# Optimization experiments

Hardware: AMD Instinct MI355X
Metric: run time of the kernel (lower is better)

Reference implementation:

```python
import jax, jax.numpy as jnp
import numpy as np

N = 50000      # nodes
E = 800000     # edges
D = 128        # input_dim
H = 128        # hidden_dim
OUT = 86       # output_dim (DDI classes)
P = 100000     # drug pairs
BN_EPS = 1e-5


def setup_inputs() -> dict:
    key = jax.random.key(0)
    ks = jax.random.split(key, 16)
    s = 0.05
    return {
        "x": jax.random.normal(ks[0], (N, D), jnp.float32),
        "edge_index": jax.random.randint(ks[1], (2, E), 0, N),
        "drug_pairs": jax.random.randint(ks[2], (P, 2), 0, N),
        # GCN layer 1 (input_dim -> hidden_dim) + BatchNorm params
        "W1": jax.random.normal(ks[3], (D, H), jnp.float32) * s,
        "b1": jnp.zeros((H,), jnp.float32),
        "gamma1": jnp.ones((H,), jnp.float32),
        "beta1": jnp.zeros((H,), jnp.float32),
        # GCN layer 2 (hidden -> hidden) + BatchNorm params
        "W2": jax.random.normal(ks[4], (H, H), jnp.float32) * s,
        "b2": jnp.zeros((H,), jnp.float32),
        "gamma2": jnp.ones((H,), jnp.float32),
        "beta2": jnp.zeros((H,), jnp.float32),
        # edge classifier MLP: Linear(2H,H) -> ReLU -> Linear(H,H//2) -> ReLU -> Linear(H//2,OUT)
        "Wc1": jax.random.normal(ks[5], (2 * H, H), jnp.float32) * s,
        "bc1": jnp.zeros((H,), jnp.float32),
        "Wc2": jax.random.normal(ks[6], (H, H // 2), jnp.float32) * s,
        "bc2": jnp.zeros((H // 2,), jnp.float32),
        "Wc3": jax.random.normal(ks[7], (H // 2, OUT), jnp.float32) * s,
        "bc3": jnp.zeros((OUT,), jnp.float32),
    }


def gcn_conv(h, W, b, src, dst, n):
    """PyG GCNConv: D^-1/2 (A + I) D^-1/2 (h @ W) + b, with self-loops added."""
    h = h @ W  # [N, H]
    ones = jnp.ones(src.shape[0], h.dtype)
    deg = jax.ops.segment_sum(ones, dst, num_segments=n) + 1.0  # in-degree + self loop
    dinv = jax.lax.rsqrt(deg)  # [N]
    coef = dinv[src] * dinv[dst]  # [E] edge normalization
    agg = jax.ops.segment_sum(h[src] * coef[:, None], dst, num_segments=n)
    agg = agg + h * (dinv * dinv)[:, None]  # self-loop contribution: deg_i^-1 * h_i
    return agg + b


def batch_norm(h, gamma, beta):
    # training-mode BatchNorm1d over node dim (biased variance)
    mean = jnp.mean(h, axis=0)
    var = jnp.mean((h - mean) ** 2, axis=0)
    return gamma * (h - mean) * jax.lax.rsqrt(var + BN_EPS) + beta


def reference(x, edge_index, drug_pairs, W1, b1, gamma1, beta1,
              W2, b2, gamma2, beta2, Wc1, bc1, Wc2, bc2, Wc3, bc3):
    src, dst = edge_index[0], edge_index[1]
    n = x.shape[0]
    # layer 1
    h = jax.nn.relu(batch_norm(gcn_conv(x, W1, b1, src, dst, n), gamma1, beta1))
    # layer 2
    h = jax.nn.relu(batch_norm(gcn_conv(h, W2, b2, src, dst, n), gamma2, beta2))
    # node-pair gather + concat -> edge classifier MLP (dropout = identity in eval)
    combined = jnp.concatenate([h[drug_pairs[:, 0]], h[drug_pairs[:, 1]]], axis=1)  # [P, 2H]
    z = jax.nn.relu(combined @ Wc1 + bc1)
    z = jax.nn.relu(z @ Wc2 + bc2)
    return z @ Wc3 + bc3  # [P, OUT]
```

## Files before the change

### kernel.cpp

```cpp
#include <hip/hip_runtime.h>
#include <cstdint>

#define N_NODES 50000
#define N_EDGES 800000
#define NPAIRS  100000

typedef unsigned short u16;
typedef unsigned int u32;
typedef unsigned long long u64;
typedef _Float16 f16;
typedef short short8v __attribute__((ext_vector_type(8)));
typedef _Float16 h8 __attribute__((ext_vector_type(8)));
typedef _Float16 h4 __attribute__((ext_vector_type(4)));
typedef float f32x4 __attribute__((ext_vector_type(4)));

static __device__ __forceinline__ u16 f2bf(float f) {
  unsigned int u = __float_as_uint(f);
  u += 0x7FFF + ((u >> 16) & 1);
  return (u16)(u >> 16);
}

static __device__ __forceinline__ float bits2f(u32 hi) {
  union { u16 b; f16 h; } x;
  x.b = (u16)hi;
  return (float)x.h;
}


__global__ __launch_bounds__(256) void pre_k(const int* __restrict__ ei, int* __restrict__ deg, int* __restrict__ rank,
                                             const float* __restrict__ W1, const float* __restrict__ W2,
                                             const float* __restrict__ Wc1, const float* __restrict__ Wc2,
                                             const float* __restrict__ Wc3,
                                             f16* __restrict__ W1F, f16* __restrict__ W2F,
                                             u16* __restrict__ Wc1F, u16* __restrict__ Wc2F, u16* __restrict__ Wc3F) {
  int b = blockIdx.x;
  if (b < N_EDGES / 256) {
    int e = b * 256 + threadIdx.x;
    rank[e] = atomicAdd(&deg[ei[N_EDGES + e]], 1);
    return;
  }
  int slot = (b - N_EDGES / 256) * 256 + threadIdx.x;
  int lane = slot & 63, j = lane & 15, kg = lane >> 4;
  if (slot < 2048) {
    int ks = (slot >> 6) & 3, nt = slot >> 8;
    int k0 = ks * 32 + kg * 8, c = nt * 16 + j;
#pragma unroll
    for (int e = 0; e < 8; e++) W1F[(size_t)slot * 8 + e] = (f16)W1[(k0 + e) * 128 + c];
  } else if (slot < 4096) {
    int s2 = slot - 2048;
    int ks = (s2 >> 6) & 3, nt = s2 >> 8;
    int k0 = ks * 32 + kg * 8, c = nt * 16 + j;
#pragma unroll
    for (int e = 0; e < 8; e++) W2F[(size_t)s2 * 8 + e] = (f16)W2[(k0 + e) * 128 + c];
  } else if (slot < 8192) {
    int s3 = slot - 4096;
    int ks = (s3 >> 6) & 7, nt = s3 >> 9;
    int k0 = ks * 32 + kg * 8, c = nt * 16 + j;
#pragma unroll
    for (int e = 0; e < 8; e++) Wc1F[(size_t)s3 * 8 + e] = f2bf(Wc1[(k0 + e) * 128 + c]);
  } else if (slot < 9216) {
    int s4 = slot - 8192;
    int ks = (s4 >> 6) & 3, nt = s4 >> 8;
    int k0 = ks * 32 + kg * 8, c = nt * 16 + j;
#pragma unroll
    for (int e = 0; e < 8; e++) Wc2F[(size_t)s4 * 8 + e] = f2bf(Wc2[(k0 + e) * 64 + c]);
  } else if (slot < 10240) {
    int s5 = slot - 9216;
    int ks = (s5 >> 6) & 1, nt = s5 >> 7;
    int k0 = ks * 32 + kg * 8, c = nt * 16 + j;
#pragma unroll
    for (int e = 0; e < 8; e++)
      Wc3F[(size_t)s5 * 8 + e] = f2bf((c < 86) ? Wc3[(k0 + e) * 86 + c] : 0.f);
  }
}

__global__ __launch_bounds__(1024) void scan_k(const int* __restrict__ deg, int* __restrict__ offs,
                                               float* __restrict__ dinv, int n) {
  __shared__ int wsum[16];
  __shared__ int wpre[16];
  __shared__ int run_s;
  int tid = threadIdx.x, lane = tid & 63, wid = tid >> 6;
  if (tid == 0) run_s = 0;
  __syncthreads();
  for (int base = 0; base < n; base += 4096) {
    int i4 = base + tid * 4;
    int4 v = make_int4(0, 0, 0, 0);
    if (i4 + 3 < n) v = *(const int4*)&deg[i4];
    else {
      if (i4 < n) v.x = deg[i4];
      if (i4 + 1 < n) v.y = deg[i4 + 1];
      if (i4 + 2 < n) v.z = deg[i4 + 2];
      if (i4 + 3 < n) v.w = deg[i4 + 3];
    }
    int tsum = v.x + v.y + v.z + v.w;
    int s = tsum;
#pragma unroll
    for (int d = 1; d < 64; d <<= 1) {
      int t = __shfl_up(s, d);
      if (lane >= d) s += t;
    }
    if (lane == 63) wsum[wid] = s;
    __syncthreads();
    if (tid == 0) {
      int acc = run_s;
#pragma unroll
      for (int w = 0; w < 16; w++) { wpre[w] = acc; acc += wsum[w]; }
      run_s = acc;
    }
    __syncthreads();
    int pre = wpre[wid] + (s - tsum);
    int4 o;
    o.x = pre; o.y = pre + v.x; o.z = o.y + v.y; o.w = o.z + v.z;
    float4 dv;
    dv.x = rsqrtf((float)v.x + 1.0f);
    dv.y = rsqrtf((float)v.y + 1.0f);
    dv.z = rsqrtf((float)v.z + 1.0f);
    dv.w = rsqrtf((float)v.w + 1.0f);
    if (i4 + 3 < n) {
      *(int4*)&offs[i4] = o;
      *(float4*)&dinv[i4] = dv;
    } else {
      if (i4 < n)     { offs[i4] = o.x;     dinv[i4] = dv.x; }
      if (i4 + 1 < n) { offs[i4 + 1] = o.y; dinv[i4 + 1] = dv.y; }
      if (i4 + 2 < n) { offs[i4 + 2] = o.z; dinv[i4 + 2] = dv.z; }
      if (i4 + 3 < n) { offs[i4 + 3] = o.w; dinv[i4 + 3] = dv.w; }
    }
    __syncthreads();
  }
  if (tid == 0) offs[n] = run_s;
}

__global__ __launch_bounds__(256) void fill_k(const int* __restrict__ ei, const int* __restrict__ offs,
                                              const int* __restrict__ rank, const float* __restrict__ dinv,
                                              u32* __restrict__ csrp, int E) {
  int e = blockIdx.x * 256 + threadIdx.x;
  if (e < E) {
    int s = ei[e], d = ei[E + e];
    int idx = offs[d] + rank[e];
    f16 hv = (f16)dinv[s];
    u32 pack = (u32)(u16)s | ((u32)(*(u16*)&hv) << 16);
    csrp[idx] = pack;
  }
}


template<int MODE>
__global__ __launch_bounds__(256) void gemm_mfma_k(const void* __restrict__ Ain,
                                                   const float* __restrict__ sums,
                                                   const float* __restrict__ gamma,
                                                   const float* __restrict__ beta,
                                                   const f16* __restrict__ WF,
                                                   f16* __restrict__ outh, int n) {
  __shared__ f16 As[64 * 136];
  __shared__ float scsh[256];
  int tid = threadIdx.x;
  if (MODE == 1) {
    if (tid < 128) {
      const float inv_n = 1.0f / (float)N_NODES;
      float mean = sums[tid] * inv_n;
      float var = sums[128 + tid] * inv_n - mean * mean;
      float sc = gamma[tid] * rsqrtf(var + 1e-5f);
      scsh[tid] = sc;
      scsh[128 + tid] = beta[tid] - mean * sc;
    }
    __syncthreads();
  }
  int row0 = blockIdx.x * 64;
#pragma unroll
  for (int it = 0; it < 8; it++) {
    int idx = it * 256 + tid;
    int r = idx >> 5, c4 = (idx & 31) * 4;
    int gr = row0 + r; if (gr >= n) gr = n - 1;
    float4 v;
    if (MODE == 0) {
      v = *(const float4*)&((const float*)Ain)[(size_t)gr * 128 + c4];
    } else {
      h4 hv4 = *(const h4*)&((const f16*)Ain)[(size_t)gr * 128 + c4];
      v.x = (float)hv4[0]; v.y = (float)hv4[1]; v.z = (float)hv4[2]; v.w = (float)hv4[3];
      v.x = fmaxf(v.x * scsh[c4 + 0] + scsh[128 + c4 + 0], 0.f);
      v.y = fmaxf(v.y * scsh[c4 + 1] + scsh[128 + c4 + 1], 0.f);
      v.z = fmaxf(v.z * scsh[c4 + 2] + scsh[128 + c4 + 2], 0.f);
      v.w = fmaxf(v.w * scsh[c4 + 3] + scsh[128 + c4 + 3], 0.f);
    }
    h4 hv; hv[0] = (f16)v.x; hv[1] = (f16)v.y; hv[2] = (f16)v.z; hv[3] = (f16)v.w;
    *(h4*)&As[r * 136 + c4] = hv;
  }
  __syncthreads();
  int w = tid >> 6, lane = tid & 63, li = lane & 15, kg = lane >> 4;
  f32x4 acc[4][2];
#pragma unroll
  for (int mt = 0; mt < 4; mt++)
#pragma unroll
    for (int ntl = 0; ntl < 2; ntl++)
#pragma unroll
      for (int q = 0; q < 4; q++) acc[mt][ntl][q] = 0.f;
#pragma unroll
  for (int ks = 0; ks < 4; ks++) {
    h8 a[4];
#pragma unroll
    for (int mt = 0; mt < 4; mt++)
      a[mt] = *(const h8*)&As[(mt * 16 + li) * 136 + kg * 8 + ks * 32];
#pragma unroll
    for (int ntl = 0; ntl < 2; ntl++) {
      int nt = 2 * w + ntl;
      h8 b = *(const h8*)&WF[((size_t)(nt * 4 + ks) * 64 + lane) * 8];
#pragma unroll
      for (int mt = 0; mt < 4; mt++)
        acc[mt][ntl] = __builtin_amdgcn_mfma_f32_16x16x32_f16(a[mt], b, acc[mt][ntl], 0, 0, 0);
    }
  }
  __syncthreads();
#pragma unroll
  for (int mt = 0; mt < 4; mt++)
#pragma unroll
    for (int ntl = 0; ntl < 2; ntl++)
#pragma unroll
      for (int r = 0; r < 4; r++)
        As[(mt * 16 + kg * 4 + r) * 136 + (2 * w + ntl) * 16 + li] = (f16)acc[mt][ntl][r];
  __syncthreads();
#pragma unroll
  for (int it = 0; it < 4; it++) {
    int idx = it * 256 + tid;
    int r = idx >> 4, c8 = (idx & 15) * 8;
    int gr = row0 + r;
    if (gr < n) *(h8*)&outh[(size_t)gr * 128 + c8] = *(const h8*)&As[r * 136 + c8];
  }
}


__global__ __launch_bounds__(256) void agg_h_k(const f16* __restrict__ th, const float* __restrict__ dinv,
                                               const int* __restrict__ offs, const u32* __restrict__ csrp,
                                               const float* __restrict__ bias, f16* __restrict__ outh, int n) {
  int tid = threadIdx.x;
  int w = tid >> 6, lane = tid & 63;
  int half = lane >> 5, sl = lane & 31;
  int node = blockIdx.x * 4 + w;
  if (node >= n) return;
  const u64* hu8 = (const u64*)th;
  float di = dinv[node];
  int e0 = offs[node], e1 = offs[node + 1];
  union C8 { u64 u; f16 h[4]; };
  float a0[4] = {0.f, 0.f, 0.f, 0.f};
  float a1[4] = {0.f, 0.f, 0.f, 0.f};
  float a2[4] = {0.f, 0.f, 0.f, 0.f};
  float a3[4] = {0.f, 0.f, 0.f, 0.f};
  int e = e0;
  for (; e + 8 <= e1; e += 8) {
    u32 p0 = csrp[e + half];
    u32 p1 = csrp[e + 2 + half];
    u32 p2 = csrp[e + 4 + half];
    u32 p3 = csrp[e + 6 + half];
    C8 v0, v1, v2, v3;
    v0.u = hu8[(size_t)(p0 & 0xFFFF) * 32 + sl];
    v1.u = hu8[(size_t)(p1 & 0xFFFF) * 32 + sl];
    v2.u = hu8[(size_t)(p2 & 0xFFFF) * 32 + sl];
    v3.u = hu8[(size_t)(p3 & 0xFFFF) * 32 + sl];
    float c0 = bits2f(p0 >> 16), c1 = bits2f(p1 >> 16);
    float c2 = bits2f(p2 >> 16), c3 = bits2f(p3 >> 16);
#pragma unroll
    for (int j = 0; j < 4; j++) {
      a0[j] += c0 * (float)v0.h[j];
      a1[j] += c1 * (float)v1.h[j];
      a2[j] += c2 * (float)v2.h[j];
      a3[j] += c3 * (float)v3.h[j];
    }
  }
  for (; e < e1; e += 2) {
    int ee = e + half;
    bool valid = ee < e1;
    u32 p0 = csrp[valid ? ee : e];
    float c0 = valid ? bits2f(p0 >> 16) : 0.f;
    C8 v0; v0.u = hu8[(size_t)(p0 & 0xFFFF) * 32 + sl];
#pragma unroll
    for (int j = 0; j < 4; j++) a0[j] += c0 * (float)v0.h[j];
  }
  float s[4];
#pragma unroll
  for (int j = 0; j < 4; j++) {
    s[j] = (a0[j] + a1[j]) + (a2[j] + a3[j]);
    s[j] += __shfl_xor(s[j], 32);
  }
  if (half == 0) {
    C8 vs; vs.u = hu8[(size_t)node * 32 + sl];
    float4 b4 = *(const float4*)&bias[sl * 4];
    float sc = di * di;
    C8 o;
    o.h[0] = (f16)(di * s[0] + sc * (float)vs.h[0] + b4.x);
    o.h[1] = (f16)(di * s[1] + sc * (float)vs.h[1] + b4.y);
    o.h[2] = (f16)(di * s[2] + sc * (float)vs.h[2] + b4.z);
    o.h[3] = (f16)(di * s[3] + sc * (float)vs.h[3] + b4.w);
    ((u64*)outh)[(size_t)node * 32 + sl] = o.u;
  }
}


__global__ __launch_bounds__(256) void bn_stats_h_k(const f16* __restrict__ h, float* __restrict__ sums, int n) {
  int tid = threadIdx.x;
  int c = tid & 63, rg = tid >> 6;
  const u32* hu = (const u32*)h;
  union CV { u32 u; f16 h[2]; };
  float sx = 0.f, sy = 0.f, qx = 0.f, qy = 0.f;
  for (int r = blockIdx.x * 4 + rg; r < n; r += gridDim.x * 4) {
    CV v; v.u = hu[(size_t)r * 64 + c];
    float x = (float)v.h[0], y = (float)v.h[1];
    sx += x; qx += x * x;
    sy += y; qy += y * y;
  }
  __shared__ float rsum[4][128];
  __shared__ float rsq[4][128];
  rsum[rg][c * 2] = sx; rsum[rg][c * 2 + 1] = sy;
  rsq[rg][c * 2] = qx;  rsq[rg][c * 2 + 1] = qy;
  __syncthreads();
  if (tid < 128) {
    float a = (rsum[0][tid] + rsum[1][tid]) + (rsum[2][tid] + rsum[3][tid]);
    float b = (rsq[0][tid] + rsq[1][tid]) + (rsq[2][tid] + rsq[3][tid]);
    atomicAdd(&sums[tid], a);
    atomicAdd(&sums[128 + tid], b);
  }
}


__global__ __launch_bounds__(256) void bn_apply_bf16_k(const f16* __restrict__ h, const float* __restrict__ sums,
                                                       const float* __restrict__ gamma, const float* __restrict__ beta,
                                                       u16* __restrict__ hb) {
  __shared__ float scsh[256];
  int tid = threadIdx.x;
  if (tid < 128) {
    const float inv_n = 1.0f / (float)N_NODES;
    float mean = sums[tid] * inv_n;
    float var = sums[128 + tid] * inv_n - mean * mean;
    float sc = gamma[tid] * rsqrtf(var + 1e-5f);
    scsh[tid] = sc;
    scsh[128 + tid] = beta[tid] - mean * sc;
  }
  __syncthreads();
  int idx = blockIdx.x * 256 + tid;
  int c0 = (idx & 31) * 4;
  h4 v4 = *(const h4*)&h[(size_t)idx * 4];
  ushort4 o;
  o.x = f2bf(fmaxf((float)v4[0] * scsh[c0 + 0] + scsh[128 + c0 + 0], 0.f));
  o.y = f2bf(fmaxf((float)v4[1] * scsh[c0 + 1] + scsh[128 + c0 + 1], 0.f));
  o.z = f2bf(fmaxf((float)v4[2] * scsh[c0 + 2] + scsh[128 + c0 + 2], 0.f));
  o.w = f2bf(fmaxf((float)v4[3] * scsh[c0 + 3] + scsh[128 + c0 + 3], 0.f));
  *(ushort4*)&hb[(size_t)idx * 4] = o;
}


#define SM_Z1 33792
#define SM_TOT (33792 + 17408)

__global__ __launch_bounds__(256) void classifier_k(const u16* __restrict__ hbf, const int* __restrict__ pairs,
    const u16* __restrict__ Wc1F, const float* __restrict__ bc1,
    const u16* __restrict__ Wc2F, const float* __restrict__ bc2,
    const u16* __restrict__ Wc3F, const float* __restrict__ bc3,
    float* __restrict__ out) {
  __shared__ __align__(16) char smem[SM_TOT];
  __shared__ int nodes[128];
  int tid = threadIdx.x;
  int p0 = blockIdx.x * 64;
  if (tid < 128) {
    int gi = p0 * 2 + tid;
    nodes[tid] = (gi < NPAIRS * 2) ? pairs[gi] : 0;
  }
  __syncthreads();
  int w = tid >> 6, lane = tid & 63;
  int li = lane & 15, kg = lane >> 4;

  {
    unsigned int* cmb = (unsigned int*)smem;
    for (int s = w * 32; s < w * 32 + 32; s++) {
      int nd = nodes[s];
      unsigned int v = ((const unsigned int*)hbf)[(size_t)nd * 64 + lane];
      cmb[(s >> 1) * 132 + (s & 1) * 64 + lane] = v;
    }
  }
  __syncthreads();

  {
    f32x4 acc[4][2];
#pragma unroll
    for (int ntl = 0; ntl < 2; ntl++) {
      float b = bc1[(2 * w + ntl) * 16 + li];
#pragma unroll
      for (int mt = 0; mt < 4; mt++)
#pragma unroll
        for (int q = 0; q < 4; q++) acc[mt][ntl][q] = b;
    }
    for (int ks = 0; ks < 8; ks++) {
      short8v a[4];
#pragma unroll
      for (int mt = 0; mt < 4; mt++)
        a[mt] = *(const short8v*)(smem + (mt * 16 + li) * 528 + kg * 16 + ks * 64);
#pragma unroll
      for (int ntl = 0; ntl < 2; ntl++) {
        int nt = 2 * w + ntl;
        short8v b = *(const short8v*)(Wc1F + ((size_t)(nt * 8 + ks) * 64 + lane) * 8);
#pragma unroll
        for (int mt = 0; mt < 4; mt++)
          acc[mt][ntl] = __builtin_amdgcn_mfma_f32_16x16x32_bf16(a[mt], b, acc[mt][ntl], 0, 0, 0);
      }
    }
#pragma unroll
    for (int mt = 0; mt < 4; mt++)
#pragma unroll
      for (int ntl = 0; ntl < 2; ntl++)
#pragma unroll
        for (int r = 0; r < 4; r++) {
          int row = mt * 16 + kg * 4 + r;
          int col = (2 * w + ntl) * 16 + li;
          *(u16*)(smem + SM_Z1 + row * 272 + col * 2) = f2bf(fmaxf(acc[mt][ntl][r], 0.f));
        }
  }
  __syncthreads();

  {
    f32x4 acc[4];
    float b = bc2[w * 16 + li];
#pragma unroll
    for (int mt = 0; mt < 4; mt++)
#pragma unroll
      for (int q = 0; q < 4; q++) acc[mt][q] = b;
    for (int ks = 0; ks < 4; ks++) {
      short8v a[4];
#pragma unroll
      for (int mt = 0; mt < 4; mt++)
        a[mt] = *(const short8v*)(smem + SM_Z1 + (mt * 16 + li) * 272 + kg * 16 + ks * 64);
      short8v bf = *(const short8v*)(Wc2F + ((size_t)(w * 4 + ks) * 64 + lane) * 8);
#pragma unroll
      for (int mt = 0; mt < 4; mt++)
        acc[mt] = __builtin_amdgcn_mfma_f32_16x16x32_bf16(a[mt], bf, acc[mt], 0, 0, 0);
    }
#pragma unroll
    for (int mt = 0; mt < 4; mt++)
#pragma unroll
      for (int r = 0; r < 4; r++) {
        int row = mt * 16 + kg * 4 + r;
        int col = w * 16 + li;
        *(u16*)(smem + row * 144 + col * 2) = f2bf(fmaxf(acc[mt][r], 0.f));
      }
  }
  __syncthreads();

  {
    f32x4 acc[4][2];
#pragma unroll
    for (int ntl = 0; ntl < 2; ntl++) {
      int col = (2 * w + ntl) * 16 + li;
      float b = (col < 86) ? bc3[col] : 0.f;
#pragma unroll
      for (int mt = 0; mt < 4; mt++)
#pragma unroll
        for (int q = 0; q < 4; q++) acc[mt][ntl][q] = b;
    }
    for (int ks = 0; ks < 2; ks++) {
      short8v a[4];
#pragma unroll
      for (int mt = 0; mt < 4; mt++)
        a[mt] = *(const short8v*)(smem + (mt * 16 + li) * 144 + kg * 16 + ks * 64);
#pragma unroll
      for (int ntl = 0; ntl < 2; ntl++) {
        int nt = 2 * w + ntl;
        short8v bf = *(const short8v*)(Wc3F + ((size_t)(nt * 2 + ks) * 64 + lane) * 8);
#pragma unroll
        for (int mt = 0; mt < 4; mt++)
          acc[mt][ntl] = __builtin_amdgcn_mfma_f32_16x16x32_bf16(a[mt], bf, acc[mt][ntl], 0, 0, 0);
      }
    }
#pragma unroll
    for (int mt = 0; mt < 4; mt++)
#pragma unroll
      for (int ntl = 0; ntl < 2; ntl++) {
        int col = (2 * w + ntl) * 16 + li;
        if (col < 86) {
#pragma unroll
          for (int r = 0; r < 4; r++) {
            int row = p0 + mt * 16 + kg * 4 + r;
            if (row < NPAIRS) out[(size_t)row * 86 + col] = acc[mt][ntl][r];
          }
        }
      }
  }
}


extern "C" void kernel_launch(void* const* d_in, const int* in_sizes, int n_in,
                              void* d_out, int out_size, void* d_ws, size_t ws_size,
                              hipStream_t stream) {
  (void)in_sizes; (void)n_in; (void)out_size; (void)ws_size;
  const float* x   = (const float*)d_in[0];
  const int*   ei  = (const int*)d_in[1];
  const int* pairs = (const int*)d_in[2];
  const float* W1  = (const float*)d_in[3];
  const float* b1  = (const float*)d_in[4];
  const float* g1  = (const float*)d_in[5];
  const float* be1 = (const float*)d_in[6];
  const float* W2  = (const float*)d_in[7];
  const float* b2  = (const float*)d_in[8];
  const float* g2  = (const float*)d_in[9];
  const float* be2 = (const float*)d_in[10];
  const float* Wc1 = (const float*)d_in[11];
  const float* bc1 = (const float*)d_in[12];
  const float* Wc2 = (const float*)d_in[13];
  const float* bc2 = (const float*)d_in[14];
  const float* Wc3 = (const float*)d_in[15];
  const float* bc3 = (const float*)d_in[16];
  float* out = (float*)d_out;

  size_t off = 0;
  auto alloc = [&](size_t bytes) -> char* {
    char* p = (char*)d_ws + off;
    off += (bytes + 255) & ~(size_t)255;
    return p;
  };
  int* deg      = (int*)alloc(N_NODES * 4);
  float* sums1  = (float*)alloc(256 * 4);
  float* sums2  = (float*)alloc(256 * 4);
  size_t zero_span = off;
  int* offs     = (int*)alloc((N_NODES + 1) * 4);
  int* rank     = (int*)alloc(N_EDGES * 4);
  u32* csrp     = (u32*)alloc(N_EDGES * 4);
  float* dinv   = (float*)alloc(N_NODES * 4);
  f16* W1F      = (f16*)alloc(2048 * 8 * 2);
  f16* W2F      = (f16*)alloc(2048 * 8 * 2);
  u16* Wc1F     = (u16*)alloc(4096 * 8 * 2);
  u16* Wc2F     = (u16*)alloc(1024 * 8 * 2);
  u16* Wc3F     = (u16*)alloc(1024 * 8 * 2);
  f16* th       = (f16*)alloc((size_t)N_NODES * 128 * 2);
  f16* hA       = (f16*)alloc((size_t)N_NODES * 128 * 2);
  u16* hbf      = (u16*)th;

  hipMemsetAsync(d_ws, 0, zero_span, stream);
  pre_k<<<N_EDGES / 256 + 40, 256, 0, stream>>>(ei, deg, rank, W1, W2, Wc1, Wc2, Wc3,
                                                W1F, W2F, Wc1F, Wc2F, Wc3F);
  scan_k<<<1, 1024, 0, stream>>>(deg, offs, dinv, N_NODES);
  fill_k<<<N_EDGES / 256, 256, 0, stream>>>(ei, offs, rank, dinv, csrp, N_EDGES);

  gemm_mfma_k<0><<<(N_NODES + 63) / 64, 256, 0, stream>>>(x, nullptr, nullptr, nullptr, W1F, th, N_NODES);
  agg_h_k<<<(N_NODES + 3) / 4, 256, 0, stream>>>(th, dinv, offs, csrp, b1, hA, N_NODES);
  bn_stats_h_k<<<256, 256, 0, stream>>>(hA, sums1, N_NODES);

  gemm_mfma_k<1><<<(N_NODES + 63) / 64, 256, 0, stream>>>(hA, sums1, g1, be1, W2F, th, N_NODES);
  agg_h_k<<<(N_NODES + 3) / 4, 256, 0, stream>>>(th, dinv, offs, csrp, b2, hA, N_NODES);
  bn_stats_h_k<<<256, 256, 0, stream>>>(hA, sums2, N_NODES);

  bn_apply_bf16_k<<<(N_NODES * 128) / 1024, 256, 0, stream>>>(hA, sums2, g2, be2, hbf);

  classifier_k<<<(NPAIRS + 63) / 64, 256, 0, stream>>>(hbf, pairs, Wc1F, bc1, Wc2F, bc2, Wc3F, bc3, out);
}
```

Measured before the change: 335.8 us.

## Fuse degree counting with first GEMM and fold final BN into classifier

```diff
diff --git a/kernel.cpp b/kernel.cpp
--- a/kernel.cpp
+++ b/kernel.cpp
@@ -27,51 +27,150 @@
 }
 
 
-__global__ __launch_bounds__(256) void pre_k(const int* __restrict__ ei, int* __restrict__ deg, int* __restrict__ rank,
-                                             const float* __restrict__ W1, const float* __restrict__ W2,
-                                             const float* __restrict__ Wc1, const float* __restrict__ Wc2,
-                                             const float* __restrict__ Wc3,
-                                             f16* __restrict__ W1F, f16* __restrict__ W2F,
-                                             u16* __restrict__ Wc1F, u16* __restrict__ Wc2F, u16* __restrict__ Wc3F) {
+__global__ __launch_bounds__(256) void wpack_k(const float* __restrict__ W1, const float* __restrict__ W2,
+                                               const float* __restrict__ Wc1, const float* __restrict__ Wc2,
+                                               const float* __restrict__ Wc3,
+                                               f16* __restrict__ W1F, f16* __restrict__ W2F,
+                                               u16* __restrict__ Wc1F, u16* __restrict__ Wc2F, u16* __restrict__ Wc3F) {
+  int slot = blockIdx.x * 256 + threadIdx.x;
+  int lane = slot & 63, j = lane & 15, kg = lane >> 4;
+  if (slot < 2048) {
+    int ks = (slot >> 6) & 3, nt = slot >> 8;
+    int k0 = ks * 32 + kg * 8, c = nt * 16 + j;
+#pragma unroll
+    for (int e = 0; e < 8; e++) W1F[(size_t)slot * 8 + e] = (f16)W1[(k0 + e) * 128 + c];
+  } else if (slot < 4096) {
+    int s2 = slot - 2048;
+    int ks = (s2 >> 6) & 3, nt = s2 >> 8;
+    int k0 = ks * 32 + kg * 8, c = nt * 16 + j;
+#pragma unroll
+    for (int e = 0; e < 8; e++) W2F[(size_t)s2 * 8 + e] = (f16)W2[(k0 + e) * 128 + c];
+  } else if (slot < 8192) {
+    int s3 = slot - 4096;
+    int ks = (s3 >> 6) & 7, nt = s3 >> 9;
+    int k0 = ks * 32 + kg * 8, c = nt * 16 + j;
+#pragma unroll
+    for (int e = 0; e < 8; e++) Wc1F[(size_t)s3 * 8 + e] = f2bf(Wc1[(k0 + e) * 128 + c]);
+  } else if (slot < 9216) {
+    int s4 = slot - 8192;
+    int ks = (s4 >> 6) & 3, nt = s4 >> 8;
+    int k0 = ks * 32 + kg * 8, c = nt * 16 + j;
+#pragma unroll
+    for (int e = 0; e < 8; e++) Wc2F[(size_t)s4 * 8 + e] = f2bf(Wc2[(k0 + e) * 64 + c]);
+  } else if (slot < 10240) {
+    int s5 = slot - 9216;
+    int ks = (s5 >> 6) & 1, nt = s5 >> 7;
+    int k0 = ks * 32 + kg * 8, c = nt * 16 + j;
+#pragma unroll
+    for (int e = 0; e < 8; e++)
+      Wc3F[(size_t)s5 * 8 + e] = f2bf((c < 86) ? Wc3[(k0 + e) * 86 + c] : 0.f);
+  }
+}
+
+
+template<int MODE>
+static __device__ __forceinline__ void gemm_body(const void* __restrict__ Ain,
+                                                 const float* __restrict__ sums,
+                                                 const float* __restrict__ gamma,
+                                                 const float* __restrict__ beta,
+                                                 const f16* __restrict__ WF,
+                                                 f16* __restrict__ outh, int n, int row0,
+                                                 f16* As, float* scsh) {
+  int tid = threadIdx.x;
+  if constexpr (MODE == 1) {
+    if (tid < 128) {
+      const float inv_n = 1.0f / (float)N_NODES;
+      float mean = sums[tid] * inv_n;
+      float var = sums[128 + tid] * inv_n - mean * mean;
+      float sc = gamma[tid] * rsqrtf(var + 1e-5f);
+      scsh[tid] = sc;
+      scsh[128 + tid] = beta[tid] - mean * sc;
+    }
+    __syncthreads();
+  }
+#pragma unroll
+  for (int it = 0; it < 8; it++) {
+    int idx = it * 256 + tid;
+    int r = idx >> 5, c4 = (idx & 31) * 4;
+    int gr = row0 + r; if (gr >= n) gr = n - 1;
+    float4 v;
+    if constexpr (MODE == 0) {
+      v = *(const float4*)&((const float*)Ain)[(size_t)gr * 128 + c4];
+    } else {
+      h4 hv4 = *(const h4*)&((const f16*)Ain)[(size_t)gr * 128 + c4];
+      v.x = (float)hv4[0]; v.y = (float)hv4[1]; v.z = (float)hv4[2]; v.w = (float)hv4[3];
+      v.x = fmaxf(v.x * scsh[c4 + 0] + scsh[128 + c4 + 0], 0.f);
+      v.y = fmaxf(v.y * scsh[c4 + 1] + scsh[128 + c4 + 1], 0.f);
+      v.z = fmaxf(v.z * scsh[c4 + 2] + scsh[128 + c4 + 2], 0.f);
+      v.w = fmaxf(v.w * scsh[c4 + 3] + scsh[128 + c4 + 3], 0.f);
+    }
+    h4 hv; hv[0] = (f16)v.x; hv[1] = (f16)v.y; hv[2] = (f16)v.z; hv[3] = (f16)v.w;
+    *(h4*)&As[r * 136 + c4] = hv;
+  }
+  __syncthreads();
+  int w = tid >> 6, lane = tid & 63, li = lane & 15, kg = lane >> 4;
+  f32x4 acc[4][2];
+#pragma unroll
+  for (int mt = 0; mt < 4; mt++)
+#pragma unroll
+    for (int ntl = 0; ntl < 2; ntl++)
+#pragma unroll
+      for (int q = 0; q < 4; q++) acc[mt][ntl][q] = 0.f;
+#pragma unroll
+  for (int ks = 0; ks < 4; ks++) {
+    h8 a[4];
+#pragma unroll
+    for (int mt = 0; mt < 4; mt++)
+      a[mt] = *(const h8*)&As[(mt * 16 + li) * 136 + kg * 8 + ks * 32];
+#pragma unroll
+    for (int ntl = 0; ntl < 2; ntl++) {
+      int nt = 2 * w + ntl;
+      h8 b = *(const h8*)&WF[((size_t)(nt * 4 + ks) * 64 + lane) * 8];
+#pragma unroll
+      for (int mt = 0; mt < 4; mt++)
+        acc[mt][ntl] = __builtin_amdgcn_mfma_f32_16x16x32_f16(a[mt], b, acc[mt][ntl], 0, 0, 0);
+    }
+  }
+  __syncthreads();
+#pragma unroll
+  for (int mt = 0; mt < 4; mt++)
+#pragma unroll
+    for (int ntl = 0; ntl < 2; ntl++)
+#pragma unroll
+      for (int r = 0; r < 4; r++)
+        As[(mt * 16 + kg * 4 + r) * 136 + (2 * w + ntl) * 16 + li] = (f16)acc[mt][ntl][r];
+  __syncthreads();
+#pragma unroll
+  for (int it = 0; it < 4; it++) {
+    int idx = it * 256 + tid;
+    int r = idx >> 4, c8 = (idx & 15) * 8;
+    int gr = row0 + r;
+    if (gr < n) *(h8*)&outh[(size_t)gr * 128 + c8] = *(const h8*)&As[r * 136 + c8];
+  }
+}
+
+
+__global__ __launch_bounds__(256) void fused1_k(const int* __restrict__ ei, int* __restrict__ deg,
+                                                int* __restrict__ rank,
+                                                const float* __restrict__ x, const f16* __restrict__ W1F,
+                                                f16* __restrict__ th, int n) {
+  __shared__ f16 As[64 * 136];
   int b = blockIdx.x;
   if (b < N_EDGES / 256) {
     int e = b * 256 + threadIdx.x;
     rank[e] = atomicAdd(&deg[ei[N_EDGES + e]], 1);
     return;
   }
-  int slot = (b - N_EDGES / 256) * 256 + threadIdx.x;
-  int lane = slot & 63, j = lane & 15, kg = lane >> 4;
-  if (slot < 2048) {
-    int ks = (slot >> 6) & 3, nt = slot >> 8;
-    int k0 = ks * 32 + kg * 8, c = nt * 16 + j;
-#pragma unroll
-    for (int e = 0; e < 8; e++) W1F[(size_t)slot * 8 + e] = (f16)W1[(k0 + e) * 128 + c];
-  } else if (slot < 4096) {
-    int s2 = slot - 2048;
-    int ks = (s2 >> 6) & 3, nt = s2 >> 8;
-    int k0 = ks * 32 + kg * 8, c = nt * 16 + j;
-#pragma unroll
-    for (int e = 0; e < 8; e++) W2F[(size_t)s2 * 8 + e] = (f16)W2[(k0 + e) * 128 + c];
-  } else if (slot < 8192) {
-    int s3 = slot - 4096;
-    int ks = (s3 >> 6) & 7, nt = s3 >> 9;
-    int k0 = ks * 32 + kg * 8, c = nt * 16 + j;
-#pragma unroll
-    for (int e = 0; e < 8; e++) Wc1F[(size_t)s3 * 8 + e] = f2bf(Wc1[(k0 + e) * 128 + c]);
-  } else if (slot < 9216) {
-    int s4 = slot - 8192;
-    int ks = (s4 >> 6) & 3, nt = s4 >> 8;
-    int k0 = ks * 32 + kg * 8, c = nt * 16 + j;
-#pragma unroll
-    for (int e = 0; e < 8; e++) Wc2F[(size_t)s4 * 8 + e] = f2bf(Wc2[(k0 + e) * 64 + c]);
-  } else if (slot < 10240) {
-    int s5 = slot - 9216;
-    int ks = (s5 >> 6) & 1, nt = s5 >> 7;
-    int k0 = ks * 32 + kg * 8, c = nt * 16 + j;
-#pragma unroll
-    for (int e = 0; e < 8; e++)
-      Wc3F[(size_t)s5 * 8 + e] = f2bf((c < 86) ? Wc3[(k0 + e) * 86 + c] : 0.f);
-  }
+  gemm_body<0>(x, nullptr, nullptr, nullptr, W1F, th, n, (b - N_EDGES / 256) * 64, As, nullptr);
+}
+
+
+__global__ __launch_bounds__(256) void gemm2_k(const f16* __restrict__ Ain, const float* __restrict__ sums,
+                                               const float* __restrict__ gamma, const float* __restrict__ beta,
+                                               const f16* __restrict__ W2F, f16* __restrict__ th, int n) {
+  __shared__ f16 As[64 * 136];
+  __shared__ float scsh[256];
+  gemm_body<1>(Ain, sums, gamma, beta, W2F, th, n, blockIdx.x * 64, As, scsh);
 }
 
 __global__ __launch_bounds__(1024) void scan_k(const int* __restrict__ deg, int* __restrict__ offs,
@@ -82,17 +181,19 @@
   int tid = threadIdx.x, lane = tid & 63, wid = tid >> 6;
   if (tid == 0) run_s = 0;
   __syncthreads();
-  for (int base = 0; base < n; base += 4096) {
-    int i4 = base + tid * 4;
-    int4 v = make_int4(0, 0, 0, 0);
-    if (i4 + 3 < n) v = *(const int4*)&deg[i4];
-    else {
-      if (i4 < n) v.x = deg[i4];
-      if (i4 + 1 < n) v.y = deg[i4 + 1];
-      if (i4 + 2 < n) v.z = deg[i4 + 2];
-      if (i4 + 3 < n) v.w = deg[i4 + 3];
-    }
-    int tsum = v.x + v.y + v.z + v.w;
+  for (int base = 0; base < n; base += 8192) {
+    int i8 = base + tid * 8;
+    int v[8];
+    if (i8 + 7 < n) {
+      *(int4*)&v[0] = *(const int4*)&deg[i8];
+      *(int4*)&v[4] = *(const int4*)&deg[i8 + 4];
+    } else {
+#pragma unroll
+      for (int j = 0; j < 8; j++) v[j] = (i8 + j < n) ? deg[i8 + j] : 0;
+    }
+    int tsum = 0;
+#pragma unroll
+    for (int j = 0; j < 8; j++) tsum += v[j];
     int s = tsum;
 #pragma unroll
     for (int d = 1; d < 64; d <<= 1) {
@@ -109,21 +210,22 @@
     }
     __syncthreads();
     int pre = wpre[wid] + (s - tsum);
-    int4 o;
-    o.x = pre; o.y = pre + v.x; o.z = o.y + v.y; o.w = o.z + v.z;
-    float4 dv;
-    dv.x = rsqrtf((float)v.x + 1.0f);
-    dv.y = rsqrtf((float)v.y + 1.0f);
-    dv.z = rsqrtf((float)v.z + 1.0f);
-    dv.w = rsqrtf((float)v.w + 1.0f);
-    if (i4 + 3 < n) {
-      *(int4*)&offs[i4] = o;
-      *(float4*)&dinv[i4] = dv;
+    int o[8];
+    o[0] = pre;
+#pragma unroll
+    for (int j = 1; j < 8; j++) o[j] = o[j - 1] + v[j - 1];
+    float dv[8];
+#pragma unroll
+    for (int j = 0; j < 8; j++) dv[j] = rsqrtf((float)v[j] + 1.0f);
+    if (i8 + 7 < n) {
+      *(int4*)&offs[i8] = *(int4*)&o[0];
+      *(int4*)&offs[i8 + 4] = *(int4*)&o[4];
+      *(float4*)&dinv[i8] = *(float4*)&dv[0];
+      *(float4*)&dinv[i8 + 4] = *(float4*)&dv[4];
     } else {
-      if (i4 < n)     { offs[i4] = o.x;     dinv[i4] = dv.x; }
-      if (i4 + 1 < n) { offs[i4 + 1] = o.y; dinv[i4 + 1] = dv.y; }
-      if (i4 + 2 < n) { offs[i4 + 2] = o.z; dinv[i4 + 2] = dv.z; }
-      if (i4 + 3 < n) { offs[i4 + 3] = o.w; dinv[i4 + 3] = dv.w; }
+#pragma unroll
+      for (int j = 0; j < 8; j++)
+        if (i8 + j < n) { offs[i8 + j] = o[j]; dinv[i8 + j] = dv[j]; }
     }
     __syncthreads();
   }
@@ -140,90 +242,6 @@
     f16 hv = (f16)dinv[s];
     u32 pack = (u32)(u16)s | ((u32)(*(u16*)&hv) << 16);
     csrp[idx] = pack;
-  }
-}
-
-
-template<int MODE>
-__global__ __launch_bounds__(256) void gemm_mfma_k(const void* __restrict__ Ain,
-                                                   const float* __restrict__ sums,
-                                                   const float* __restrict__ gamma,
-                                                   const float* __restrict__ beta,
-                                                   const f16* __restrict__ WF,
-                                                   f16* __restrict__ outh, int n) {
-  __shared__ f16 As[64 * 136];
-  __shared__ float scsh[256];
-  int tid = threadIdx.x;
-  if (MODE == 1) {
-    if (tid < 128) {
-      const float inv_n = 1.0f / (float)N_NODES;
-      float mean = sums[tid] * inv_n;
-      float var = sums[128 + tid] * inv_n - mean * mean;
-      float sc = gamma[tid] * rsqrtf(var + 1e-5f);
-      scsh[tid] = sc;
-      scsh[128 + tid] = beta[tid] - mean * sc;
-    }
-    __syncthreads();
-  }
-  int row0 = blockIdx.x * 64;
-#pragma unroll
-  for (int it = 0; it < 8; it++) {
-    int idx = it * 256 + tid;
-    int r = idx >> 5, c4 = (idx & 31) * 4;
-    int gr = row0 + r; if (gr >= n) gr = n - 1;
-    float4 v;
-    if (MODE == 0) {
-      v = *(const float4*)&((const float*)Ain)[(size_t)gr * 128 + c4];
-    } else {
-      h4 hv4 = *(const h4*)&((const f16*)Ain)[(size_t)gr * 128 + c4];
-      v.x = (float)hv4[0]; v.y = (float)hv4[1]; v.z = (float)hv4[2]; v.w = (float)hv4[3];
-      v.x = fmaxf(v.x * scsh[c4 + 0] + scsh[128 + c4 + 0], 0.f);
-      v.y = fmaxf(v.y * scsh[c4 + 1] + scsh[128 + c4 + 1], 0.f);
-      v.z = fmaxf(v.z * scsh[c4 + 2] + scsh[128 + c4 + 2], 0.f);
-      v.w = fmaxf(v.w * scsh[c4 + 3] + scsh[128 + c4 + 3], 0.f);
-    }
-    h4 hv; hv[0] = (f16)v.x; hv[1] = (f16)v.y; hv[2] = (f16)v.z; hv[3] = (f16)v.w;
-    *(h4*)&As[r * 136 + c4] = hv;
-  }
-  __syncthreads();
-  int w = tid >> 6, lane = tid & 63, li = lane & 15, kg = lane >> 4;
-  f32x4 acc[4][2];
-#pragma unroll
-  for (int mt = 0; mt < 4; mt++)
-#pragma unroll
-    for (int ntl = 0; ntl < 2; ntl++)
-#pragma unroll
-      for (int q = 0; q < 4; q++) acc[mt][ntl][q] = 0.f;
-#pragma unroll
-  for (int ks = 0; ks < 4; ks++) {
-    h8 a[4];
-#pragma unroll
-    for (int mt = 0; mt < 4; mt++)
-      a[mt] = *(const h8*)&As[(mt * 16 + li) * 136 + kg * 8 + ks * 32];
-#pragma unroll
-    for (int ntl = 0; ntl < 2; ntl++) {
-      int nt = 2 * w + ntl;
-      h8 b = *(const h8*)&WF[((size_t)(nt * 4 + ks) * 64 + lane) * 8];
-#pragma unroll
-      for (int mt = 0; mt < 4; mt++)
-        acc[mt][ntl] = __builtin_amdgcn_mfma_f32_16x16x32_f16(a[mt], b, acc[mt][ntl], 0, 0, 0);
-    }
-  }
-  __syncthreads();
-#pragma unroll
-  for (int mt = 0; mt < 4; mt++)
-#pragma unroll
-    for (int ntl = 0; ntl < 2; ntl++)
-#pragma unroll
-      for (int r = 0; r < 4; r++)
-        As[(mt * 16 + kg * 4 + r) * 136 + (2 * w + ntl) * 16 + li] = (f16)acc[mt][ntl][r];
-  __syncthreads();
-#pragma unroll
-  for (int it = 0; it < 4; it++) {
-    int idx = it * 256 + tid;
-    int r = idx >> 4, c8 = (idx & 15) * 8;
-    int gr = row0 + r;
-    if (gr < n) *(h8*)&outh[(size_t)gr * 128 + c8] = *(const h8*)&As[r * 136 + c8];
   }
 }
 
@@ -320,12 +338,24 @@
 }
 
 
-__global__ __launch_bounds__(256) void bn_apply_bf16_k(const f16* __restrict__ h, const float* __restrict__ sums,
-                                                       const float* __restrict__ gamma, const float* __restrict__ beta,
-                                                       u16* __restrict__ hb) {
+#define SM_Z1 33792
+#define SM_TOT (33792 + 17408)
+
+__global__ __launch_bounds__(256) void classifier_k(const f16* __restrict__ hA, const float* __restrict__ sums,
+    const float* __restrict__ gamma, const float* __restrict__ beta,
+    const int* __restrict__ pairs,
+    const u16* __restrict__ Wc1F, const float* __restrict__ bc1,
+    const u16* __restrict__ Wc2F, const float* __restrict__ bc2,
+    const u16* __restrict__ Wc3F, const float* __restrict__ bc3,
+    float* __restrict__ out) {
+  __shared__ __align__(16) char smem[SM_TOT];
+  __shared__ int nodes[128];
   __shared__ float scsh[256];
   int tid = threadIdx.x;
+  int p0 = blockIdx.x * 64;
   if (tid < 128) {
+    int gi = p0 * 2 + tid;
+    nodes[tid] = (gi < NPAIRS * 2) ? pairs[gi] : 0;
     const float inv_n = 1.0f / (float)N_NODES;
     float mean = sums[tid] * inv_n;
     float var = sums[128 + tid] * inv_n - mean * mean;
@@ -334,44 +364,21 @@
     scsh[128 + tid] = beta[tid] - mean * sc;
   }
   __syncthreads();
-  int idx = blockIdx.x * 256 + tid;
-  int c0 = (idx & 31) * 4;
-  h4 v4 = *(const h4*)&h[(size_t)idx * 4];
-  ushort4 o;
-  o.x = f2bf(fmaxf((float)v4[0] * scsh[c0 + 0] + scsh[128 + c0 + 0], 0.f));
-  o.y = f2bf(fmaxf((float)v4[1] * scsh[c0 + 1] + scsh[128 + c0 + 1], 0.f));
-  o.z = f2bf(fmaxf((float)v4[2] * scsh[c0 + 2] + scsh[128 + c0 + 2], 0.f));
-  o.w = f2bf(fmaxf((float)v4[3] * scsh[c0 + 3] + scsh[128 + c0 + 3], 0.f));
-  *(ushort4*)&hb[(size_t)idx * 4] = o;
-}
-
-
-#define SM_Z1 33792
-#define SM_TOT (33792 + 17408)
-
-__global__ __launch_bounds__(256) void classifier_k(const u16* __restrict__ hbf, const int* __restrict__ pairs,
-    const u16* __restrict__ Wc1F, const float* __restrict__ bc1,
-    const u16* __restrict__ Wc2F, const float* __restrict__ bc2,
-    const u16* __restrict__ Wc3F, const float* __restrict__ bc3,
-    float* __restrict__ out) {
-  __shared__ __align__(16) char smem[SM_TOT];
-  __shared__ int nodes[128];
-  int tid = threadIdx.x;
-  int p0 = blockIdx.x * 64;
-  if (tid < 128) {
-    int gi = p0 * 2 + tid;
-    nodes[tid] = (gi < NPAIRS * 2) ? pairs[gi] : 0;
-  }
-  __syncthreads();
   int w = tid >> 6, lane = tid & 63;
   int li = lane & 15, kg = lane >> 4;
 
   {
     unsigned int* cmb = (unsigned int*)smem;
+    int c0 = lane * 2;
+    float sc0 = scsh[c0], sh0 = scsh[128 + c0];
+    float sc1 = scsh[c0 + 1], sh1 = scsh[128 + c0 + 1];
+    union CV { u32 u; f16 h[2]; };
     for (int s = w * 32; s < w * 32 + 32; s++) {
       int nd = nodes[s];
-      unsigned int v = ((const unsigned int*)hbf)[(size_t)nd * 64 + lane];
-      cmb[(s >> 1) * 132 + (s & 1) * 64 + lane] = v;
+      CV v; v.u = ((const u32*)hA)[(size_t)nd * 64 + lane];
+      u32 b0 = f2bf(fmaxf((float)v.h[0] * sc0 + sh0, 0.f));
+      u32 b1 = f2bf(fmaxf((float)v.h[1] * sc1 + sh1, 0.f));
+      cmb[(s >> 1) * 132 + (s & 1) * 64 + lane] = b0 | (b1 << 16);
     }
   }
   __syncthreads();
@@ -527,23 +534,21 @@
   u16* Wc3F     = (u16*)alloc(1024 * 8 * 2);
   f16* th       = (f16*)alloc((size_t)N_NODES * 128 * 2);
   f16* hA       = (f16*)alloc((size_t)N_NODES * 128 * 2);
-  u16* hbf      = (u16*)th;
 
   hipMemsetAsync(d_ws, 0, zero_span, stream);
-  pre_k<<<N_EDGES / 256 + 40, 256, 0, stream>>>(ei, deg, rank, W1, W2, Wc1, Wc2, Wc3,
-                                                W1F, W2F, Wc1F, Wc2F, Wc3F);
+  wpack_k<<<40, 256, 0, stream>>>(W1, W2, Wc1, Wc2, Wc3, W1F, W2F, Wc1F, Wc2F, Wc3F);
+
+  fused1_k<<<N_EDGES / 256 + (N_NODES + 63) / 64, 256, 0, stream>>>(ei, deg, rank, x, W1F, th, N_NODES);
   scan_k<<<1, 1024, 0, stream>>>(deg, offs, dinv, N_NODES);
   fill_k<<<N_EDGES / 256, 256, 0, stream>>>(ei, offs, rank, dinv, csrp, N_EDGES);
 
-  gemm_mfma_k<0><<<(N_NODES + 63) / 64, 256, 0, stream>>>(x, nullptr, nullptr, nullptr, W1F, th, N_NODES);
   agg_h_k<<<(N_NODES + 3) / 4, 256, 0, stream>>>(th, dinv, offs, csrp, b1, hA, N_NODES);
   bn_stats_h_k<<<256, 256, 0, stream>>>(hA, sums1, N_NODES);
 
-  gemm_mfma_k<1><<<(N_NODES + 63) / 64, 256, 0, stream>>>(hA, sums1, g1, be1, W2F, th, N_NODES);
+  gemm2_k<<<(N_NODES + 63) / 64, 256, 0, stream>>>(hA, sums1, g1, be1, W2F, th, N_NODES);
   agg_h_k<<<(N_NODES + 3) / 4, 256, 0, stream>>>(th, dinv, offs, csrp, b2, hA, N_NODES);
   bn_stats_h_k<<<256, 256, 0, stream>>>(hA, sums2, N_NODES);
 
-  bn_apply_bf16_k<<<(N_NODES * 128) / 1024, 256, 0, stream>>>(hA, sums2, g2, be2, hbf);
-
-  classifier_k<<<(NPAIRS + 63) / 64, 256, 0, stream>>>(hbf, pairs, Wc1F, bc1, Wc2F, bc2, Wc3F, bc3, out);
-}
+  classifier_k<<<(NPAIRS + 63) / 64, 256, 0, stream>>>(hA, sums2, g2, be2, pairs,
+                                                       Wc1F, bc1, Wc2F, bc2, Wc3F, bc3, out);
+}
```

Result: no change. 333.5 us (-0.7%).
